# Optimization experiments

Hardware: AMD Instinct MI355X
Metric: run time of the kernel (lower is better)

Reference implementation:

```python
import jax, jax.numpy as jnp
import numpy as np

MARGIN = 1.0  # configs: COSINE_DISTANCE=True, INVERTED_LOSS=True
EPS = 1e-8


def setup_inputs() -> dict:
    key = jax.random.key(0)
    B, d = 8192, 128
    inputs = jax.random.normal(key, (B, d), dtype=jnp.float32)
    return {"inputs": inputs}


def reference(inputs):
    B = inputs.shape[0]
    P = B // 2
    # inverted cosine distance: D = X X^T / 128
    D = jnp.matmul(inputs, inputs.T) / 128.0          # [B, B]
    Dexpm = jnp.exp(MARGIN + D)                       # [B, B]

    # rows pos_i = 2p gather odd columns 2k+1; rows pos_j = 2p+1 gather even columns 2l
    E_io = Dexpm[0::2, 1::2]                          # [P, P]
    E_je = Dexpm[1::2, 0::2]                          # [P, P]

    p = jnp.arange(P)
    k = jnp.arange(P)
    # faithful to original: exclude k == pos_j (=2p+1) and l == pos_i (=2p)
    mask_i = k[None, :] != (2 * p + 1)[:, None]       # [P, P]
    mask_j = k[None, :] != (2 * p)[:, None]           # [P, P]

    neg_ik = jnp.sum(jnp.where(mask_i, E_io, 0.0), axis=1)  # [P]
    neg_jl = jnp.sum(jnp.where(mask_j, E_je, 0.0), axis=1)  # [P]

    D_pos = D[2 * p, 2 * p + 1]                       # [P]
    J = jnp.log(EPS + neg_ik + neg_jl) - D_pos        # inverted loss: log(Dissim) - D_pos
    return jnp.sum(jnp.square(jnp.maximum(J, 0.0))) / B
```

## Files before the change

### kernel.cpp

```cpp
#include <hip/hip_runtime.h>
#include <hip/hip_bf16.h>
#include <math.h>

#define P 4096
#define DIM 128
#define MARGIN_F 1.0f
#define EPS_F 1e-8f

#define ROWS_PER_BLOCK 64
#define COLS_PER_BLOCK 256
#define TILE_COLS 64
#define NTILES 4

typedef float f32x4 __attribute__((ext_vector_type(4)));
typedef short bf16x8 __attribute__((ext_vector_type(8)));

static __device__ __forceinline__ void gload_lds16(const void* g, void* l) {
    __builtin_amdgcn_global_load_lds(
        (const __attribute__((address_space(1))) void*)g,
        (__attribute__((address_space(3))) void*)l,
        16, 0, 0);
}

__global__ __launch_bounds__(256) void convert_deint(
    const float* __restrict__ x,
    short* __restrict__ xe,
    short* __restrict__ xo,
    float* __restrict__ rowcol,
    float* __restrict__ out) {

    const int idx = blockIdx.x * 256 + threadIdx.x;
    const int row = idx >> 5;
    const int c4 = idx & 31;

    f32x4 v = *reinterpret_cast<const f32x4*>(x + (size_t)idx * 4);
    const bool odd = row & 1;
    const float s = odd ? 1.0f : 0.0078125f;
    short4 pk;
    pk.x = __builtin_bit_cast(short, __float2bfloat16(v[0] * s));
    pk.y = __builtin_bit_cast(short, __float2bfloat16(v[1] * s));
    pk.z = __builtin_bit_cast(short, __float2bfloat16(v[2] * s));
    pk.w = __builtin_bit_cast(short, __float2bfloat16(v[3] * s));
    short* dst = odd ? xo : xe;
    *reinterpret_cast<short4*>(&dst[(size_t)(row >> 1) * DIM + c4 * 4]) = pk;

    if (idx < 2 * P) rowcol[idx] = 0.0f;
    if (idx == 0) out[0] = 0.0f;
}

__global__ __launch_bounds__(256, 4) void gram_mfma(
    const short* __restrict__ xe,
    const short* __restrict__ xo,
    float* __restrict__ rowsum,
    float* __restrict__ colsum) {

    __shared__ __align__(16) short Bs[2][TILE_COLS * DIM];
    __shared__ float cs_lds[4][COLS_PER_BLOCK];

    const int tid = threadIdx.x;
    const int lane = tid & 63;
    const int wave = tid >> 6;
    const int p0 = blockIdx.y * ROWS_PER_BLOCK;
    const int c0 = blockIdx.x * COLS_PER_BLOCK;
    const int lrow = lane & 15;
    const int kgrp = (lane >> 4) * 8;

    for (int i = tid; i < 4 * COLS_PER_BLOCK; i += 256)
        (&cs_lds[0][0])[i] = 0.0f;

    const char* gB = (const char*)(xo + (size_t)c0 * DIM);
    auto stage = [&](int t) {
        char* lB = (char*)Bs[t & 1];
        const char* gt = gB + (size_t)t * (TILE_COLS * DIM * 2);
        #pragma unroll
        for (int i = 0; i < 4; ++i) {
            int Lbase = (wave * 4 + i) * 1024;
            int L = Lbase + lane * 16;
            int src = L ^ (((L >> 8) & 7) << 4);
            gload_lds16(gt + src, lB + Lbase);
        }
    };
    stage(0);

    bf16x8 a[4];
    {
        const short* arow = xe + (size_t)(p0 + wave * 16 + lrow) * DIM + kgrp;
        #pragma unroll
        for (int k32 = 0; k32 < 4; ++k32)
            a[k32] = *reinterpret_cast<const bf16x8*>(arow + k32 * 32);
    }

    float rs[4] = {0.f, 0.f, 0.f, 0.f};

    for (int t = 0; t < NTILES; ++t) {
        __syncthreads();
        if (t + 1 < NTILES) stage(t + 1);

        const short* B = Bs[t & 1];
        f32x4 acc[4];
        #pragma unroll
        for (int n = 0; n < 4; ++n) acc[n] = f32x4{0.f, 0.f, 0.f, 0.f};

        #pragma unroll
        for (int k32 = 0; k32 < 4; ++k32) {
            #pragma unroll
            for (int n = 0; n < 4; ++n) {
                int cc = n * 16 + lrow;
                int idx = (cc * DIM + k32 * 32 + kgrp) ^ ((cc & 7) << 3);
                bf16x8 b = *reinterpret_cast<const bf16x8*>(&B[idx]);
                acc[n] = __builtin_amdgcn_mfma_f32_16x16x32_bf16(
                    a[k32], b, acc[n], 0, 0, 0);
            }
        }

        #pragma unroll
        for (int n = 0; n < 4; ++n) {
            float cp = 0.0f;
            #pragma unroll
            for (int j = 0; j < 4; ++j) {
                float e = __expf(MARGIN_F + acc[n][j]);
                rs[j] += e;
                cp += e;
            }
            cp += __shfl_xor(cp, 16);
            cp += __shfl_xor(cp, 32);
            if (lane < 16)
                cs_lds[wave][t * TILE_COLS + n * 16 + lane] += cp;
        }
    }

    #pragma unroll
    for (int j = 0; j < 4; ++j) {
        float v = rs[j];
        v += __shfl_xor(v, 1);
        v += __shfl_xor(v, 2);
        v += __shfl_xor(v, 4);
        v += __shfl_xor(v, 8);
        rs[j] = v;
    }
    if (lrow == 0) {
        int g = lane >> 4;
        #pragma unroll
        for (int j = 0; j < 4; ++j)
            atomicAdd(&rowsum[p0 + wave * 16 + g * 4 + j], rs[j]);
    }

    __syncthreads();
    float s = cs_lds[0][tid] + cs_lds[1][tid] + cs_lds[2][tid] + cs_lds[3][tid];
    atomicAdd(&colsum[c0 + tid], s);
}

__global__ __launch_bounds__(256) void finalize(
    const float* __restrict__ x,
    const float* __restrict__ rowsum,
    const float* __restrict__ colsum,
    float* __restrict__ out) {

    __shared__ float wsum[4];
    const int tid = threadIdx.x;
    const int wave = tid >> 6;
    const int lane = tid & 63;

    float racc = 0.0f;
    #pragma unroll
    for (int q = 0; q < 4; ++q) {
        const int p = blockIdx.x * 16 + wave * 4 + q;

        const float2* xep = reinterpret_cast<const float2*>(x + (size_t)(2 * p) * DIM);
        const float2* xop = reinterpret_cast<const float2*>(x + (size_t)(2 * p + 1) * DIM);
        float2 ve = xep[lane];
        float2 vo = xop[lane];
        float dpos = ve.x * vo.x + ve.y * vo.y;

        float ci = 0.0f, cj = 0.0f;
        if (p < P / 2) {
            const float2* xi = reinterpret_cast<const float2*>(x + (size_t)(4 * p + 3) * DIM);
            const float2* xj = reinterpret_cast<const float2*>(x + (size_t)(4 * p) * DIM);
            float2 vi = xi[lane];
            float2 vj = xj[lane];
            ci = ve.x * vi.x + ve.y * vi.y;
            cj = vo.x * vj.x + vo.y * vj.y;
        }

        #pragma unroll
        for (int off = 32; off > 0; off >>= 1) {
            dpos += __shfl_down(dpos, off);
            ci   += __shfl_down(ci, off);
            cj   += __shfl_down(cj, off);
        }

        if (lane == 0) {
            float corr = 0.0f;
            if (p < P / 2)
                corr = __expf(MARGIN_F + ci * (1.0f / 128.0f))
                     + __expf(MARGIN_F + cj * (1.0f / 128.0f));
            float neg = rowsum[p] + colsum[p] - corr;
            float J = logf(EPS_F + neg) - dpos * (1.0f / 128.0f);
            float r = fmaxf(J, 0.0f);
            racc += r * r;
        }
    }

    if (lane == 0) wsum[wave] = racc;
    __syncthreads();
    if (tid == 0) {
        float s = (wsum[0] + wsum[1] + wsum[2] + wsum[3]) * (1.0f / 8192.0f);
        atomicAdd(out, s);
    }
}

extern "C" void kernel_launch(void* const* d_in, const int* in_sizes, int n_in,
                              void* d_out, int out_size, void* d_ws, size_t ws_size,
                              hipStream_t stream) {
    const float* x = (const float*)d_in[0];
    float* rowsum = (float*)d_ws;
    float* colsum = rowsum + P;
    short* xe = (short*)(colsum + P);
    short* xo = xe + (size_t)P * DIM;

    convert_deint<<<1024, 256, 0, stream>>>(x, xe, xo, rowsum, (float*)d_out);
    dim3 grid(P / COLS_PER_BLOCK, P / ROWS_PER_BLOCK);
    gram_mfma<<<grid, 256, 0, stream>>>(xe, xo, rowsum, colsum);
    finalize<<<P / 16, 256, 0, stream>>>(x, rowsum, colsum, (float*)d_out);
}
```

Before: 29.41 us.

## Double rows per block in gram kernel and drop LDS column-sum staging

Each wave now computes two 16-row MFMA tiles that share every B fragment read from LDS, so the block covers 128 rows and the grid halves. Column partial sums are kept in registers per tile and pushed straight to global with atomics instead of going through an LDS buffer and a final barrier. The cost is more registers per thread (occupancy hint lowered to 2), fewer blocks to fill the GPU, and four times as many colsum atomics per block.

```diff
diff --git a/kernel.cpp b/kernel.cpp
--- a/kernel.cpp
+++ b/kernel.cpp
@@ -7,7 +7,7 @@
 #define MARGIN_F 1.0f
 #define EPS_F 1e-8f
 
-#define ROWS_PER_BLOCK 64
+#define ROWS_PER_BLOCK 128
 #define COLS_PER_BLOCK 256
 #define TILE_COLS 64
 #define NTILES 4
@@ -48,14 +48,13 @@
     if (idx == 0) out[0] = 0.0f;
 }
 
-__global__ __launch_bounds__(256, 4) void gram_mfma(
+__global__ __launch_bounds__(256, 2) void gram_mfma(
     const short* __restrict__ xe,
     const short* __restrict__ xo,
     float* __restrict__ rowsum,
     float* __restrict__ colsum) {
 
     __shared__ __align__(16) short Bs[2][TILE_COLS * DIM];
-    __shared__ float cs_lds[4][COLS_PER_BLOCK];
 
     const int tid = threadIdx.x;
     const int lane = tid & 63;
@@ -65,9 +64,6 @@
     const int lrow = lane & 15;
     const int kgrp = (lane >> 4) * 8;
 
-    for (int i = tid; i < 4 * COLS_PER_BLOCK; i += 256)
-        (&cs_lds[0][0])[i] = 0.0f;
-
     const char* gB = (const char*)(xo + (size_t)c0 * DIM);
     auto stage = [&](int t) {
         char* lB = (char*)Bs[t & 1];
@@ -82,24 +78,38 @@
     };
     stage(0);
 
-    bf16x8 a[4];
-    {
-        const short* arow = xe + (size_t)(p0 + wave * 16 + lrow) * DIM + kgrp;
+    bf16x8 a[2][4];
+    #pragma unroll
+    for (int m = 0; m < 2; ++m) {
+        const short* arow =
+            xe + (size_t)(p0 + wave * 32 + m * 16 + lrow) * DIM + kgrp;
         #pragma unroll
         for (int k32 = 0; k32 < 4; ++k32)
-            a[k32] = *reinterpret_cast<const bf16x8*>(arow + k32 * 32);
-    }
-
-    float rs[4] = {0.f, 0.f, 0.f, 0.f};
-
+            a[m][k32] = *reinterpret_cast<const bf16x8*>(arow + k32 * 32);
+    }
+
+    float rs[2][4];
+    float cpp[NTILES][4];
+    #pragma unroll
+    for (int m = 0; m < 2; ++m)
+        #pragma unroll
+        for (int j = 0; j < 4; ++j) rs[m][j] = 0.0f;
+    #pragma unroll
+    for (int t = 0; t < NTILES; ++t)
+        #pragma unroll
+        for (int n = 0; n < 4; ++n) cpp[t][n] = 0.0f;
+
+    #pragma unroll
     for (int t = 0; t < NTILES; ++t) {
         __syncthreads();
         if (t + 1 < NTILES) stage(t + 1);
 
         const short* B = Bs[t & 1];
-        f32x4 acc[4];
-        #pragma unroll
-        for (int n = 0; n < 4; ++n) acc[n] = f32x4{0.f, 0.f, 0.f, 0.f};
+        f32x4 acc[2][4];
+        #pragma unroll
+        for (int m = 0; m < 2; ++m)
+            #pragma unroll
+            for (int n = 0; n < 4; ++n) acc[m][n] = f32x4{0.f, 0.f, 0.f, 0.f};
 
         #pragma unroll
         for (int k32 = 0; k32 < 4; ++k32) {
@@ -108,46 +118,56 @@
                 int cc = n * 16 + lrow;
                 int idx = (cc * DIM + k32 * 32 + kgrp) ^ ((cc & 7) << 3);
                 bf16x8 b = *reinterpret_cast<const bf16x8*>(&B[idx]);
-                acc[n] = __builtin_amdgcn_mfma_f32_16x16x32_bf16(
-                    a[k32], b, acc[n], 0, 0, 0);
+                #pragma unroll
+                for (int m = 0; m < 2; ++m)
+                    acc[m][n] = __builtin_amdgcn_mfma_f32_16x16x32_bf16(
+                        a[m][k32], b, acc[m][n], 0, 0, 0);
             }
         }
 
         #pragma unroll
-        for (int n = 0; n < 4; ++n) {
-            float cp = 0.0f;
-            #pragma unroll
-            for (int j = 0; j < 4; ++j) {
-                float e = __expf(MARGIN_F + acc[n][j]);
-                rs[j] += e;
-                cp += e;
-            }
-            cp += __shfl_xor(cp, 16);
-            cp += __shfl_xor(cp, 32);
-            if (lane < 16)
-                cs_lds[wave][t * TILE_COLS + n * 16 + lane] += cp;
-        }
-    }
-
-    #pragma unroll
-    for (int j = 0; j < 4; ++j) {
-        float v = rs[j];
-        v += __shfl_xor(v, 1);
-        v += __shfl_xor(v, 2);
-        v += __shfl_xor(v, 4);
-        v += __shfl_xor(v, 8);
-        rs[j] = v;
-    }
+        for (int n = 0; n < 4; ++n)
+            #pragma unroll
+            for (int m = 0; m < 2; ++m)
+                #pragma unroll
+                for (int j = 0; j < 4; ++j) {
+                    float e = __expf(MARGIN_F + acc[m][n][j]);
+                    rs[m][j] += e;
+                    cpp[t][n] += e;
+                }
+    }
+
+    #pragma unroll
+    for (int m = 0; m < 2; ++m)
+        #pragma unroll
+        for (int j = 0; j < 4; ++j) {
+            float v = rs[m][j];
+            v += __shfl_xor(v, 1);
+            v += __shfl_xor(v, 2);
+            v += __shfl_xor(v, 4);
+            v += __shfl_xor(v, 8);
+            rs[m][j] = v;
+        }
     if (lrow == 0) {
         int g = lane >> 4;
         #pragma unroll
-        for (int j = 0; j < 4; ++j)
-            atomicAdd(&rowsum[p0 + wave * 16 + g * 4 + j], rs[j]);
-    }
-
-    __syncthreads();
-    float s = cs_lds[0][tid] + cs_lds[1][tid] + cs_lds[2][tid] + cs_lds[3][tid];
-    atomicAdd(&colsum[c0 + tid], s);
+        for (int m = 0; m < 2; ++m)
+            #pragma unroll
+            for (int j = 0; j < 4; ++j)
+                atomicAdd(&rowsum[p0 + wave * 32 + m * 16 + g * 4 + j],
+                          rs[m][j]);
+    }
+
+    #pragma unroll
+    for (int t = 0; t < NTILES; ++t)
+        #pragma unroll
+        for (int n = 0; n < 4; ++n) {
+            float v = cpp[t][n];
+            v += __shfl_xor(v, 16);
+            v += __shfl_xor(v, 32);
+            if (lane < 16)
+                atomicAdd(&colsum[c0 + t * TILE_COLS + n * 16 + lane], v);
+        }
 }
 
 __global__ __launch_bounds__(256) void finalize(
```

Measured after the change: 28.70 us. 1.02x faster.
